# Performance work log

Hardware: AMD Instinct MI355X
Metric: run time of the kernel (lower is better)

## Reference

```python
import jax, jax.numpy as jnp
import numpy as np

V, E, H = 32000, 1024, 1024  # vocab, wemb, enc
T1, B = 129, 64


def setup_inputs() -> dict:
    key = jax.random.key(0)
    ks = jax.random.split(key, 6)
    sH = 1.0 / np.sqrt(H)
    data = jax.random.randint(ks[0], (T1, B), 0, V)
    mask = jnp.ones((T1, B), jnp.float32)
    emb = jax.random.normal(ks[1], (V, E), jnp.float32) * 0.02
    W_ih = jax.random.normal(ks[2], (E, 4 * H), jnp.float32) * sH
    W_hh = jax.random.normal(ks[3], (H, 4 * H), jnp.float32) * sH
    b = jnp.zeros((4 * H,), jnp.float32)
    Wr = jax.random.normal(ks[4], (E, H), jnp.float32) * sH  # readout: Linear(H -> E), torch weight (out,in)
    br = jnp.zeros((E,), jnp.float32)
    bd = jnp.zeros((V,), jnp.float32)  # decoder bias (weight tied to emb)
    return {"data": data, "mask": mask, "emb": emb, "W_ih": W_ih, "W_hh": W_hh,
            "b": b, "Wr": Wr, "br": br, "bd": bd}


def reference(data, mask, emb, W_ih, W_hh, b, Wr, br, bd):
    x_data = data[:-1]          # [Tx, B]
    y_data = data[1:]           # [Tx, B]
    m_all = mask[1:]            # note: source uses mask[1:] for BOTH x_mask and y_mask
    Tx, Bn = x_data.shape

    def step(carry, xs):
        ht, ct, loss = carry
        tx, ty, mt = xs                      # [B], [B], [B]
        x = emb[tx]                          # [B, E] embedding lookup
        g = x @ W_ih + ht @ W_hh + b         # [B, 4H]
        i, f, gg, o = jnp.split(g, 4, axis=1)
        i = jax.nn.sigmoid(i); f = jax.nn.sigmoid(f); o = jax.nn.sigmoid(o)
        gg = jnp.tanh(gg)
        cn = f * ct + i * gg
        hn = o * jnp.tanh(cn)
        mm = mt[:, None]
        ht2 = mm * hn + (1.0 - mm) * ht      # masked state update
        ct2 = mm * cn + (1.0 - mm) * ct
        out = ht2 @ Wr.T + br                # readout [B, E]
        logit = out @ emb.T + bd             # tied decoder [B, V]
        logp = jax.nn.log_softmax(logit, axis=1)
        nll = -jnp.take_along_axis(logp, ty[:, None], axis=1)[:, 0]
        loss = loss + jnp.mean(nll * mt)     # loss_reduction == 'org'
        return (ht2, ct2, loss), None

    init = (jnp.zeros((Bn, H), jnp.float32), jnp.zeros((Bn, H), jnp.float32),
            jnp.zeros((), jnp.float32))
    (_, _, loss), _ = jax.lax.scan(step, init, (x_data, y_data, m_all))
    return loss / Bn
```

## Files before the change

kernel.cpp:

```cpp
#include <hip/hip_runtime.h>
#include <stdint.h>

#define V_  32000
#define E_  1024
#define H_  1024
#define B_  64
#define T_  128
#define MROWS (T_ * B_)
#define NCB_ 250
#define NTG  32
#define ITEMS_PER_TG 258
#define TOTAL_ITEMS (NTG * ITEMS_PER_TG)

typedef __bf16 bf16x8 __attribute__((ext_vector_type(8)));
typedef float  f32x4  __attribute__((ext_vector_type(4)));

__device__ __forceinline__ uint16_t f2b(float f) {
  uint32_t u = __builtin_bit_cast(uint32_t, f);
  return (uint16_t)((u + 0x7fffu + ((u >> 16) & 1u)) >> 16);
}
__device__ __forceinline__ float b2f(uint16_t h) {
  uint32_t u = ((uint32_t)h) << 16;
  return __builtin_bit_cast(float, u);
}
__device__ __forceinline__ float fsig_(float x) {
  return __builtin_amdgcn_rcpf(1.0f + __expf(-x));
}
__device__ __forceinline__ float ftanh_(float x) {
  return 2.0f * __builtin_amdgcn_rcpf(1.0f + __expf(-2.0f * x)) - 1.0f;
}

__device__ __forceinline__ void gload16(const uint16_t* g, uint16_t* l) {
  __builtin_amdgcn_global_load_lds(
      (const __attribute__((address_space(1))) uint32_t*)g,
      (__attribute__((address_space(3))) uint32_t*)l,
      16, 0, 0);
}


__global__ void k_cvt(const float* __restrict__ src, uint16_t* __restrict__ dst, int n4) {
  int i = blockIdx.x * blockDim.x + threadIdx.x;
  int st = gridDim.x * blockDim.x;
  for (; i < n4; i += st) {
    float4 v = ((const float4*)src)[i];
    ushort4 o;
    o.x = f2b(v.x); o.y = f2b(v.y); o.z = f2b(v.z); o.w = f2b(v.w);
    ((ushort4*)dst)[i] = o;
  }
}

__global__ void k_tcvt(const float* __restrict__ src, uint16_t* __restrict__ dst,
                       int R, int C, int dstStride, int dstOff) {
  __shared__ float tile[32][33];
  int c0 = blockIdx.x * 32, r0 = blockIdx.y * 32;
  int tx = threadIdx.x, ty = threadIdx.y;
  for (int j = 0; j < 32; j += 8)
    tile[ty + j][tx] = src[(size_t)(r0 + ty + j) * C + c0 + tx];
  __syncthreads();
  for (int j = 0; j < 32; j += 8)
    dst[(size_t)(c0 + ty + j) * dstStride + dstOff + r0 + tx] = f2b(tile[tx][ty + j]);
}

__global__ void k_zero(uint4* p, int n) {
  int i = blockIdx.x * blockDim.x + threadIdx.x;
  int st = gridDim.x * blockDim.x;
  uint4 z = {0, 0, 0, 0};
  for (; i < n; i += st) p[i] = z;
}

__global__ __launch_bounds__(256) void k_xw(
    const int* __restrict__ data, const uint16_t* __restrict__ embB,
    const uint16_t* __restrict__ Wcat,
    const float* __restrict__ bias, uint16_t* __restrict__ xAll)
{
  __shared__ uint16_t lA[128 * 64];
  __shared__ uint16_t lB[128 * 64];

  int tid = threadIdx.x;
  int w = tid >> 6, l = tid & 63, lr = l & 15, lg = l >> 4;
  int wr = w >> 1, wc = w & 1;
  int m0 = blockIdx.x * 128;
  int n0 = blockIdx.y * 128;

  int stRow = l >> 3;
  int kswz  = ((l & 7) * 8) ^ ((stRow & 7) << 3);
  const uint16_t* aSrc[4];
  const uint16_t* bSrc[4];
#pragma unroll
  for (int cc = 0; cc < 4; ++cc) {
    int tok = data[m0 + w * 32 + cc * 8 + stRow];
    aSrc[cc] = embB + (size_t)tok * 1024 + kswz;
    bSrc[cc] = Wcat + (size_t)(n0 + w * 32 + cc * 8 + stRow) * 2048 + kswz;
  }

  f32x4 acc[4][4] = {};

  for (int kt = 0; kt < 1024; kt += 64) {
#pragma unroll
    for (int cc = 0; cc < 4; ++cc) {
      gload16(aSrc[cc] + kt, &lA[(w * 4 + cc) * 512]);
      gload16(bSrc[cc] + kt, &lB[(w * 4 + cc) * 512]);
    }
    __syncthreads();
#pragma unroll
    for (int ksub = 0; ksub < 2; ++ksub) {
      bf16x8 af[4], bfr[4];
      int ke = ksub * 32 + lg * 8;
#pragma unroll
      for (int mi = 0; mi < 4; ++mi) {
        int row = wr * 64 + mi * 16 + lr;
        af[mi] = *(const bf16x8*)&lA[row * 64 + (ke ^ ((row & 7) << 3))];
      }
#pragma unroll
      for (int ni = 0; ni < 4; ++ni) {
        int row = wc * 64 + ni * 16 + lr;
        bfr[ni] = *(const bf16x8*)&lB[row * 64 + (ke ^ ((row & 7) << 3))];
      }
#pragma unroll
      for (int mi = 0; mi < 4; ++mi)
#pragma unroll
        for (int ni = 0; ni < 4; ++ni)
          acc[mi][ni] = __builtin_amdgcn_mfma_f32_16x16x32_bf16(af[mi], bfr[ni], acc[mi][ni], 0, 0, 0);
    }
    __syncthreads();
  }

  float bv[4];
#pragma unroll
  for (int ni = 0; ni < 4; ++ni) bv[ni] = bias[n0 + wc * 64 + ni * 16 + lr];
#pragma unroll
  for (int mi = 0; mi < 4; ++mi)
#pragma unroll
    for (int ni = 0; ni < 4; ++ni) {
      int row = wr * 64 + mi * 16 + lg * 4;
      int col = n0 + wc * 64 + ni * 16 + lr;
#pragma unroll
      for (int r = 0; r < 4; ++r)
        xAll[(size_t)(m0 + row + r) * 4096 + col] = f2b(acc[mi][ni][r] + bv[ni]);
    }
}

__global__ __launch_bounds__(512) void k_mega(
    const uint16_t* __restrict__ xAll, const uint16_t* __restrict__ Wcat,
    const float* __restrict__ mask, uint16_t* __restrict__ hAll,
    uint32_t* __restrict__ flags,
    const uint16_t* __restrict__ embB, const uint16_t* __restrict__ WrB,
    const float* __restrict__ br, const float* __restrict__ bd,
    uint16_t* __restrict__ outAll, float2* __restrict__ part,
    uint32_t* __restrict__ projDone, uint32_t* __restrict__ workCtr)
{
  __shared__ alignas(16) char smem[151616];

  int tid = threadIdx.x;
  int blk = blockIdx.x;
  int w = tid >> 6, l = tid & 63, lr = l & 15, lg = l >> 4;

  if (blk < 64) {
    uint16_t* wh    = (uint16_t*)smem;
    uint16_t* xs0   = (uint16_t*)(smem + 131072);
    uint16_t* xs1   = (uint16_t*)(smem + 139264);
    uint16_t* hp0   = (uint16_t*)(smem + 147456);
    uint16_t* hp1   = (uint16_t*)(smem + 149504);
    uint32_t* ldsT  = (uint32_t*)(smem + 151552);
    uint16_t* xsb[2] = {xs0, xs1};
    uint16_t* hpb[2] = {hp0, hp1};

    int u0 = blk * 16;

    for (int it = 0; it < 16; ++it) {
      int ch = it * 512 + tid;
      int c  = ch >> 7;
      int kb = (ch & 127) * 16;
      int gRow = (c & 3) * 1024 + u0 + (c >> 2);
      uint4 v = *(const uint4*)((const char*)Wcat + (size_t)gRow * 4096 + 2048 + kb);
      *(uint4*)((char*)wh + c * 2048 + (kb ^ ((c & 7) << 4))) = v;
    }

    int wm = w >> 1, wn = w & 1;
    int q = lr & 3;

    const char* wb0 = (const char*)wh + (size_t)(wn * 32 + lr) * 2048;
    const char* wb1 = (const char*)wh + (size_t)(wn * 32 + 16 + lr) * 2048;
    int xr = (lr & 7) << 4;

    int sRow = tid >> 3, sQ = (tid >> 1) & 3, sHalf = tid & 1;
    const uint16_t* xSrc = xAll + (size_t)sRow * 4096 + sQ * 1024 + u0 + sHalf * 8;
    int xDstOff = sRow * 64 + sQ * 16 + sHalf * 8;
    int xoBase = (wm * 16 + lg * 4) * 64 + q * 16 + wn * 8 + (lr >> 2);

    float cR[2][4] = {}, hR[2][4] = {};

    if (tid == 0) *ldsT = 0;
    *(uint4*)&xsb[0][xDstOff] = *(const uint4*)xSrc;
    __syncthreads();

    int cur = 0;
    for (int t = 0; t < T_; ++t) {
      float xwv[2][4], mm_[4];
#pragma unroll
      for (int ni = 0; ni < 2; ++ni)
#pragma unroll
        for (int r = 0; r < 4; ++r)
          xwv[ni][r] = b2f(xsb[cur][xoBase + r * 64 + ni * 4]);
#pragma unroll
      for (int r = 0; r < 4; ++r)
        mm_[r] = mask[(t + 1) * B_ + wm * 16 + lg * 4 + r];

      if (t + 1 < T_)
        *(uint4*)&xsb[cur ^ 1][xDstOff] = *(const uint4*)(xSrc + (size_t)(t + 1) * B_ * 4096);

      if (t > 0) {
        uint32_t tv = (uint32_t)t;
        if (w == 0) {
          while (!__all((int)(__hip_atomic_load(&flags[l], __ATOMIC_RELAXED,
                                                __HIP_MEMORY_SCOPE_AGENT) >= tv)))
            __builtin_amdgcn_s_sleep(1);
          __hip_atomic_store(ldsT, tv, __ATOMIC_RELEASE, __HIP_MEMORY_SCOPE_WORKGROUP);
        } else {
          while (__hip_atomic_load(ldsT, __ATOMIC_ACQUIRE,
                                   __HIP_MEMORY_SCOPE_WORKGROUP) < tv)
            __builtin_amdgcn_s_sleep(1);
        }
        asm volatile("" ::: "memory");
      }

      const uint16_t* aH = hAll + (size_t)t * (B_ * H_) + (size_t)(wm * 16 + lr) * H_ + lg * 8;

      f32x4 acc0 = {0.f, 0.f, 0.f, 0.f}, acc1 = {0.f, 0.f, 0.f, 0.f};
#pragma unroll 8
      for (int ks = 0; ks < 32; ++ks) {
        bf16x8 a = *(const bf16x8*)(aH + ks * 32);
        int ko = (ks * 64 + lg * 16) ^ xr;
        bf16x8 b0 = *(const bf16x8*)(wb0 + ko);
        bf16x8 b1 = *(const bf16x8*)(wb1 + ko);
        acc0 = __builtin_amdgcn_mfma_f32_16x16x32_bf16(a, b0, acc0, 0, 0, 0);
        acc1 = __builtin_amdgcn_mfma_f32_16x16x32_bf16(a, b1, acc1, 0, 0, 0);
      }

#pragma unroll
      for (int ni = 0; ni < 2; ++ni) {
        f32x4 accv = ni ? acc1 : acc0;
#pragma unroll
        for (int r = 0; r < 4; ++r) {
          float v0 = accv[r] + xwv[ni][r];
          float v1 = __shfl_xor(v0, 1, 64);
          float v2 = __shfl_xor(v0, 2, 64);
          float v3 = __shfl_xor(v0, 3, 64);
          float gi = (q == 0) ? v0 : (q == 1) ? v1 : (q == 2) ? v2 : v3;
          float gf = (q == 1) ? v0 : (q == 0) ? v1 : (q == 3) ? v2 : v3;
          float gg = (q == 2) ? v0 : (q == 3) ? v1 : (q == 0) ? v2 : v3;
          float go = (q == 3) ? v0 : (q == 2) ? v1 : (q == 1) ? v2 : v3;
          gi = fsig_(gi); gf = fsig_(gf); gg = ftanh_(gg); go = fsig_(go);
          float cn = gf * cR[ni][r] + gi * gg;
          float hn = go * ftanh_(cn);
          float mm = mm_[r];
          cR[ni][r] = mm * cn + (1.f - mm) * cR[ni][r];
          hR[ni][r] = mm * hn + (1.f - mm) * hR[ni][r];
          if (q == 0)
            hpb[cur][(wm * 16 + lg * 4 + r) * 16 + wn * 8 + ni * 4 + (lr >> 2)] = f2b(hR[ni][r]);
        }
      }

      __syncthreads();

      if (w == 0) {
        const unsigned long long* hp = (const unsigned long long*)hpb[cur];
        unsigned long long* hd =
            (unsigned long long*)(hAll + (size_t)(t + 1) * (B_ * H_) + (size_t)l * H_ + u0);
#pragma unroll
        for (int j = 0; j < 4; ++j)
          __hip_atomic_store(hd + j, hp[l * 4 + j],
                             __ATOMIC_RELAXED, __HIP_MEMORY_SCOPE_AGENT);
        asm volatile("s_waitcnt vmcnt(0)" ::: "memory");
        if (l == 0)
          __hip_atomic_store(&flags[blk], (uint32_t)(t + 1),
                             __ATOMIC_RELAXED, __HIP_MEMORY_SCOPE_AGENT);
      }
      cur ^= 1;
    }
  } else {
    uint16_t* lA  = (uint16_t*)smem;
    uint16_t* lB  = (uint16_t*)(smem + 32768);
    float2*   cm  = (float2*)(smem + 49152);
    uint32_t* sId = (uint32_t*)(smem + 53248);

    int stRow = l >> 3;
    int kswz  = ((l & 7) * 8) ^ ((stRow & 7) << 3);
    int wr = w >> 1;
    int wc = w & 1;

    for (;;) {
      __syncthreads();
      if (tid == 0)
        *sId = __hip_atomic_fetch_add(workCtr, 1u, __ATOMIC_RELAXED, __HIP_MEMORY_SCOPE_AGENT);
      __syncthreads();
      uint32_t id = *sId;
      if (id >= TOTAL_ITEMS) break;
      int tg = (int)(id / ITEMS_PER_TG), sub = (int)(id % ITEMS_PER_TG);
      int t0 = tg * 4;
      bool isProj = (sub < 8);

      const uint16_t* Abase;
      const uint16_t* Bbase;
      const float* biasp;
      if (isProj) {
        uint32_t tv = (uint32_t)(t0 + 4);
        while (!__all((int)(__hip_atomic_load(&flags[l], __ATOMIC_RELAXED,
                                              __HIP_MEMORY_SCOPE_AGENT) >= tv)))
          __builtin_amdgcn_s_sleep(8);
        asm volatile("" ::: "memory");
        Abase = hAll + (size_t)(t0 + 1) * (B_ * H_);
        Bbase = WrB + (size_t)(sub * 128) * 1024;
        biasp = br + sub * 128;
      } else {
        while (__hip_atomic_load(&projDone[tg], __ATOMIC_RELAXED,
                                 __HIP_MEMORY_SCOPE_AGENT) < 8u)
          __builtin_amdgcn_s_sleep(8);
        asm volatile("" ::: "memory");
        Abase = outAll + (size_t)t0 * B_ * 1024;
        Bbase = embB + (size_t)(sub - 8) * 128 * 1024;
        biasp = bd + (sub - 8) * 128;
      }

      const uint16_t* aS = Abase + (size_t)(w * 32 + stRow) * 1024 + kswz;
      const uint16_t* bS = Bbase + (size_t)(w * 16 + stRow) * 1024 + kswz;

      f32x4 acc[4][4] = {};
      for (int kt = 0; kt < 1024; kt += 64) {
#pragma unroll
        for (int cc = 0; cc < 4; ++cc)
          gload16(aS + (size_t)cc * 8 * 1024 + kt, &lA[(w * 4 + cc) * 512]);
#pragma unroll
        for (int cc = 0; cc < 2; ++cc)
          gload16(bS + (size_t)cc * 8 * 1024 + kt, &lB[(w * 2 + cc) * 512]);
        __syncthreads();
#pragma unroll
        for (int ksub = 0; ksub < 2; ++ksub) {
          int ke = ksub * 32 + lg * 8;
          bf16x8 af[4], bfr[4];
#pragma unroll
          for (int mi = 0; mi < 4; ++mi) {
            int row = wr * 64 + mi * 16 + lr;
            af[mi] = *(const bf16x8*)&lA[row * 64 + (ke ^ ((row & 7) << 3))];
          }
#pragma unroll
          for (int ni = 0; ni < 4; ++ni) {
            int row = wc * 64 + ni * 16 + lr;
            bfr[ni] = *(const bf16x8*)&lB[row * 64 + (ke ^ ((row & 7) << 3))];
          }
#pragma unroll
          for (int mi = 0; mi < 4; ++mi)
#pragma unroll
            for (int ni = 0; ni < 4; ++ni)
              acc[mi][ni] = __builtin_amdgcn_mfma_f32_16x16x32_bf16(af[mi], bfr[ni], acc[mi][ni], 0, 0, 0);
        }
        __syncthreads();
      }

      float bv[4];
#pragma unroll
      for (int ni = 0; ni < 4; ++ni) bv[ni] = biasp[wc * 64 + ni * 16 + lr];

      if (isProj) {
        int e0 = sub * 128;
        uint16_t* opack = lA;
#pragma unroll
        for (int chunk = 0; chunk < 4; ++chunk) {
          if (wr == chunk) {
#pragma unroll
            for (int mi = 0; mi < 4; ++mi)
#pragma unroll
              for (int ni = 0; ni < 4; ++ni)
#pragma unroll
                for (int r = 0; r < 4; ++r)
                  opack[(mi * 16 + lg * 4 + r) * 128 + wc * 64 + ni * 16 + lr]
                    = f2b(acc[mi][ni][r] + bv[ni]);
          }
          __syncthreads();
          const unsigned long long* op = (const unsigned long long*)opack;
#pragma unroll
          for (int j = 0; j < 4; ++j) {
            int g = j * 512 + tid;
            int row = g >> 5, seg = g & 31;
            unsigned long long* od =
                (unsigned long long*)(outAll + ((size_t)(t0 + chunk) * B_ + row) * 1024 + e0) + seg;
            __hip_atomic_store(od, op[g], __ATOMIC_RELAXED, __HIP_MEMORY_SCOPE_AGENT);
          }
          __syncthreads();
        }
        asm volatile("s_waitcnt vmcnt(0)" ::: "memory");
        __syncthreads();
        if (tid == 0)
          __hip_atomic_fetch_add(&projDone[tg], 1u, __ATOMIC_RELAXED, __HIP_MEMORY_SCOPE_AGENT);
      } else {
        int nc = sub - 8;
#pragma unroll
        for (int mi = 0; mi < 4; ++mi) {
#pragma unroll
          for (int r = 0; r < 4; ++r) {
            float mx = -1e30f;
#pragma unroll
            for (int ni = 0; ni < 4; ++ni) { acc[mi][ni][r] += bv[ni]; mx = fmaxf(mx, acc[mi][ni][r]); }
#pragma unroll
            for (int d = 1; d < 16; d <<= 1) mx = fmaxf(mx, __shfl_xor(mx, d, 64));
            float s = 0.f;
#pragma unroll
            for (int ni = 0; ni < 4; ++ni) s += expf(acc[mi][ni][r] - mx);
#pragma unroll
            for (int d = 1; d < 16; d <<= 1) s += __shfl_xor(s, d, 64);
            if (lr == 0) cm[wc * 256 + wr * 64 + mi * 16 + lg * 4 + r] = make_float2(mx, s);
          }
        }
        __syncthreads();
        if (tid < 256) {
          float2 p0 = cm[tid], p1 = cm[256 + tid];
          float M = fmaxf(p0.x, p1.x);
          float S = p0.y * expf(p0.x - M) + p1.y * expf(p1.x - M);
          part[(size_t)nc * MROWS + (size_t)t0 * B_ + tid] = make_float2(M, S);
        }
      }
    }
  }
}

__global__ __launch_bounds__(256) void k_tgt(
    const uint16_t* __restrict__ outAll, const uint16_t* __restrict__ embB,
    const float* __restrict__ bd, const int* __restrict__ data, float* __restrict__ tgt)
{
  int w = threadIdx.x >> 6, l = threadIdx.x & 63;
  int row = blockIdx.x * 4 + w;
  int t = row >> 6, b = row & 63;
  int ty = data[(t + 1) * B_ + b];
  const uint16_t* a = outAll + (size_t)row * E_;
  const uint16_t* e = embB + (size_t)ty * E_;
  float s = 0.f;
#pragma unroll
  for (int i0 = 0; i0 < 2; ++i0) {
    int i = (l + i0 * 64) * 8;
    bf16x8 av = *(const bf16x8*)(a + i);
    bf16x8 ev = *(const bf16x8*)(e + i);
#pragma unroll
    for (int j = 0; j < 8; ++j) s += (float)av[j] * (float)ev[j];
  }
#pragma unroll
  for (int d = 1; d < 64; d <<= 1) s += __shfl_xor(s, d, 64);
  if (l == 0) tgt[row] = s + bd[ty];
}

__global__ __launch_bounds__(256) void k_lse(
    const float2* __restrict__ part, const float* __restrict__ tgt,
    const float* __restrict__ mask, float* __restrict__ rowNll)
{
  int w = threadIdx.x >> 6, l = threadIdx.x & 63;
  int row = blockIdx.x * 4 + w;
  float m = -1e30f, s = 0.f;
  for (int cc = l; cc < NCB_; cc += 64) {
    float2 v = part[(size_t)cc * MROWS + row];
    float M = fmaxf(m, v.x);
    s = s * expf(m - M) + v.y * expf(v.x - M);
    m = M;
  }
#pragma unroll
  for (int d = 1; d < 64; d <<= 1) {
    float om = __shfl_xor(m, d, 64);
    float os = __shfl_xor(s, d, 64);
    float M = fmaxf(m, om);
    s = s * expf(m - M) + os * expf(om - M);
    m = M;
  }
  if (l == 0) {
    int t = row >> 6, b = row & 63;
    float nll = (m + logf(s)) - tgt[row];
    rowNll[row] = nll * mask[(t + 1) * B_ + b];
  }
}

__global__ void k_final2(const float* __restrict__ rowNll, float* __restrict__ out) {
  __shared__ float red[256];
  float s = 0.f;
  for (int i = threadIdx.x; i < MROWS; i += 256) s += rowNll[i];
  red[threadIdx.x] = s;
  __syncthreads();
  for (int st = 128; st > 0; st >>= 1) {
    if ((int)threadIdx.x < st) red[threadIdx.x] += red[threadIdx.x + st];
    __syncthreads();
  }
  if (threadIdx.x == 0) out[0] = red[0] / (float)(B_ * B_);
}

extern "C" void kernel_launch(void* const* d_in, const int* in_sizes, int n_in,
                              void* d_out, int out_size, void* d_ws, size_t ws_size,
                              hipStream_t stream)
{
  const int*   data = (const int*)  d_in[0];
  const float* mask = (const float*)d_in[1];
  const float* emb  = (const float*)d_in[2];
  const float* W_ih = (const float*)d_in[3];
  const float* W_hh = (const float*)d_in[4];
  const float* bias = (const float*)d_in[5];
  const float* Wr   = (const float*)d_in[6];
  const float* br   = (const float*)d_in[7];
  const float* bd   = (const float*)d_in[8];
  (void)in_sizes; (void)n_in; (void)out_size; (void)ws_size;

  char* ws = (char*)d_ws;
  size_t off = 0;
  auto alloc = [&](size_t bytes) -> char* {
    char* p = ws + off;
    off += (bytes + 255) & ~(size_t)255;
    return p;
  };
  uint16_t* embB   = (uint16_t*)alloc((size_t)V_ * E_ * 2);
  uint16_t* Wcat   = (uint16_t*)alloc((size_t)4 * H_ * 2048 * 2);
  uint16_t* WrB    = (uint16_t*)alloc((size_t)E_ * H_ * 2);
  uint16_t* hAll   = (uint16_t*)alloc((size_t)(T_ + 1) * B_ * H_ * 2);
  uint16_t* xAll   = (uint16_t*)alloc((size_t)MROWS * 4096 * 2);
  uint16_t* outAll = (uint16_t*)alloc((size_t)MROWS * E_ * 2);
  float2*   part   = (float2*)  alloc((size_t)NCB_ * MROWS * 8);
  float*    tgt    = (float*)   alloc((size_t)MROWS * 4);
  float*    rowNll = (float*)   alloc((size_t)MROWS * 4);
  uint32_t* syncb  = (uint32_t*)alloc(4096);
  uint32_t* flags    = syncb;
  uint32_t* projDone = syncb + 128;
  uint32_t* workCtr  = syncb + 512;

  k_cvt <<<2048, 256, 0, stream>>>(emb, embB, V_ * E_ / 4);
  k_cvt <<<256,  256, 0, stream>>>(Wr, WrB, E_ * H_ / 4);
  k_tcvt<<<dim3(4 * H_ / 32, E_ / 32), dim3(32, 8), 0, stream>>>(W_ih, Wcat, E_, 4 * H_, 2048, 0);
  k_tcvt<<<dim3(4 * H_ / 32, H_ / 32), dim3(32, 8), 0, stream>>>(W_hh, Wcat, H_, 4 * H_, 2048, 1024);
  k_zero<<<32, 256, 0, stream>>>((uint4*)hAll, B_ * H_ * 2 / 16);
  k_zero<<<1, 256, 0, stream>>>((uint4*)syncb, 4096 / 16);

  k_xw<<<dim3(MROWS / 128, 4096 / 128), 256, 0, stream>>>(data, embB, Wcat, bias, xAll);

  k_mega<<<256, 512, 0, stream>>>(xAll, Wcat, mask, hAll, flags,
                                  embB, WrB, br, bd, outAll, part,
                                  projDone, workCtr);

  k_tgt   <<<MROWS / 4, 256, 0, stream>>>(outAll, embB, bd, data, tgt);
  k_lse   <<<MROWS / 4, 256, 0, stream>>>(part, tgt, mask, rowNll);
  k_final2<<<1, 256, 0, stream>>>(rowNll, (float*)d_out);
}
```

Baseline: 1.957 ms.

## Fold input-projection GEMM into persistent megakernel as overlapped work items

Removes the separate k_xw launch and turns the x@W_ih projection into 1024 work items, each covering 256 rows by 128 columns, pulled from the megakernel's work queue ahead of the readout and decoder items. Recurrent blocks wait on per-group xwDone counters before loading each group of four timesteps' inputs, so the recurrence can start once the first group is ready instead of after the whole GEMM. Projection items now wait on a single minStep word that block 0 publishes, rather than each polling all 64 flags. The cost is more spin-waiting and the risk of stalls if the queue order delays the early x-projection groups.

Measured after the change: 1.977 ms. About the same (+1.0%).

```diff
diff --git a/kernel.cpp b/kernel.cpp
--- a/kernel.cpp
+++ b/kernel.cpp
@@ -9,8 +9,9 @@
 #define MROWS (T_ * B_)
 #define NCB_ 250
 #define NTG  32
+#define NXW  1024
 #define ITEMS_PER_TG 258
-#define TOTAL_ITEMS (NTG * ITEMS_PER_TG)
+#define TOTAL_ITEMS (NXW + NTG * ITEMS_PER_TG)
 
 typedef __bf16 bf16x8 __attribute__((ext_vector_type(8)));
 typedef float  f32x4  __attribute__((ext_vector_type(4)));
@@ -68,86 +69,17 @@
   for (; i < n; i += st) p[i] = z;
 }
 
-__global__ __launch_bounds__(256) void k_xw(
-    const int* __restrict__ data, const uint16_t* __restrict__ embB,
+__global__ __launch_bounds__(512) void k_mega(
+    const int* __restrict__ data,
+    const uint16_t* __restrict__ xAllR, uint16_t* __restrict__ xAllW,
     const uint16_t* __restrict__ Wcat,
-    const float* __restrict__ bias, uint16_t* __restrict__ xAll)
-{
-  __shared__ uint16_t lA[128 * 64];
-  __shared__ uint16_t lB[128 * 64];
-
-  int tid = threadIdx.x;
-  int w = tid >> 6, l = tid & 63, lr = l & 15, lg = l >> 4;
-  int wr = w >> 1, wc = w & 1;
-  int m0 = blockIdx.x * 128;
-  int n0 = blockIdx.y * 128;
-
-  int stRow = l >> 3;
-  int kswz  = ((l & 7) * 8) ^ ((stRow & 7) << 3);
-  const uint16_t* aSrc[4];
-  const uint16_t* bSrc[4];
-#pragma unroll
-  for (int cc = 0; cc < 4; ++cc) {
-    int tok = data[m0 + w * 32 + cc * 8 + stRow];
-    aSrc[cc] = embB + (size_t)tok * 1024 + kswz;
-    bSrc[cc] = Wcat + (size_t)(n0 + w * 32 + cc * 8 + stRow) * 2048 + kswz;
-  }
-
-  f32x4 acc[4][4] = {};
-
-  for (int kt = 0; kt < 1024; kt += 64) {
-#pragma unroll
-    for (int cc = 0; cc < 4; ++cc) {
-      gload16(aSrc[cc] + kt, &lA[(w * 4 + cc) * 512]);
-      gload16(bSrc[cc] + kt, &lB[(w * 4 + cc) * 512]);
-    }
-    __syncthreads();
-#pragma unroll
-    for (int ksub = 0; ksub < 2; ++ksub) {
-      bf16x8 af[4], bfr[4];
-      int ke = ksub * 32 + lg * 8;
-#pragma unroll
-      for (int mi = 0; mi < 4; ++mi) {
-        int row = wr * 64 + mi * 16 + lr;
-        af[mi] = *(const bf16x8*)&lA[row * 64 + (ke ^ ((row & 7) << 3))];
-      }
-#pragma unroll
-      for (int ni = 0; ni < 4; ++ni) {
-        int row = wc * 64 + ni * 16 + lr;
-        bfr[ni] = *(const bf16x8*)&lB[row * 64 + (ke ^ ((row & 7) << 3))];
-      }
-#pragma unroll
-      for (int mi = 0; mi < 4; ++mi)
-#pragma unroll
-        for (int ni = 0; ni < 4; ++ni)
-          acc[mi][ni] = __builtin_amdgcn_mfma_f32_16x16x32_bf16(af[mi], bfr[ni], acc[mi][ni], 0, 0, 0);
-    }
-    __syncthreads();
-  }
-
-  float bv[4];
-#pragma unroll
-  for (int ni = 0; ni < 4; ++ni) bv[ni] = bias[n0 + wc * 64 + ni * 16 + lr];
-#pragma unroll
-  for (int mi = 0; mi < 4; ++mi)
-#pragma unroll
-    for (int ni = 0; ni < 4; ++ni) {
-      int row = wr * 64 + mi * 16 + lg * 4;
-      int col = n0 + wc * 64 + ni * 16 + lr;
-#pragma unroll
-      for (int r = 0; r < 4; ++r)
-        xAll[(size_t)(m0 + row + r) * 4096 + col] = f2b(acc[mi][ni][r] + bv[ni]);
-    }
-}
-
-__global__ __launch_bounds__(512) void k_mega(
-    const uint16_t* __restrict__ xAll, const uint16_t* __restrict__ Wcat,
-    const float* __restrict__ mask, uint16_t* __restrict__ hAll,
-    uint32_t* __restrict__ flags,
+    const float* __restrict__ bias, const float* __restrict__ mask,
+    uint16_t* __restrict__ hAll, uint32_t* __restrict__ flags,
     const uint16_t* __restrict__ embB, const uint16_t* __restrict__ WrB,
     const float* __restrict__ br, const float* __restrict__ bd,
     uint16_t* __restrict__ outAll, float2* __restrict__ part,
-    uint32_t* __restrict__ projDone, uint32_t* __restrict__ workCtr)
+    uint32_t* __restrict__ projDone, uint32_t* __restrict__ xwDone,
+    uint32_t* __restrict__ minStep, uint32_t* __restrict__ workCtr)
 {
   __shared__ alignas(16) char smem[151616];
 
@@ -184,13 +116,16 @@
     int xr = (lr & 7) << 4;
 
     int sRow = tid >> 3, sQ = (tid >> 1) & 3, sHalf = tid & 1;
-    const uint16_t* xSrc = xAll + (size_t)sRow * 4096 + sQ * 1024 + u0 + sHalf * 8;
+    const uint16_t* xSrc = xAllR + (size_t)sRow * 4096 + sQ * 1024 + u0 + sHalf * 8;
     int xDstOff = sRow * 64 + sQ * 16 + sHalf * 8;
     int xoBase = (wm * 16 + lg * 4) * 64 + q * 16 + wn * 8 + (lr >> 2);
 
     float cR[2][4] = {}, hR[2][4] = {};
 
     if (tid == 0) *ldsT = 0;
+    while (__hip_atomic_load(&xwDone[0], __ATOMIC_RELAXED, __HIP_MEMORY_SCOPE_AGENT) < 32u)
+      __builtin_amdgcn_s_sleep(8);
+    asm volatile("" ::: "memory");
     *(uint4*)&xsb[0][xDstOff] = *(const uint4*)xSrc;
     __syncthreads();
 
@@ -206,8 +141,16 @@
       for (int r = 0; r < 4; ++r)
         mm_[r] = mask[(t + 1) * B_ + wm * 16 + lg * 4 + r];
 
-      if (t + 1 < T_)
+      if (t + 1 < T_) {
+        if (((t + 1) & 3) == 0) {
+          uint32_t g = (uint32_t)((t + 1) >> 2);
+          while (__hip_atomic_load(&xwDone[g], __ATOMIC_RELAXED,
+                                   __HIP_MEMORY_SCOPE_AGENT) < 32u)
+            __builtin_amdgcn_s_sleep(8);
+          asm volatile("" ::: "memory");
+        }
         *(uint4*)&xsb[cur ^ 1][xDstOff] = *(const uint4*)(xSrc + (size_t)(t + 1) * B_ * 4096);
+      }
 
       if (t > 0) {
         uint32_t tv = (uint32_t)t;
@@ -216,6 +159,8 @@
                                                 __HIP_MEMORY_SCOPE_AGENT) >= tv)))
             __builtin_amdgcn_s_sleep(1);
           __hip_atomic_store(ldsT, tv, __ATOMIC_RELEASE, __HIP_MEMORY_SCOPE_WORKGROUP);
+          if (blk == 0 && l == 0)
+            __hip_atomic_store(minStep, tv, __ATOMIC_RELAXED, __HIP_MEMORY_SCOPE_AGENT);
         } else {
           while (__hip_atomic_load(ldsT, __ATOMIC_ACQUIRE,
                                    __HIP_MEMORY_SCOPE_WORKGROUP) < tv)
@@ -278,6 +223,14 @@
       }
       cur ^= 1;
     }
+
+    if (blk == 0 && w == 0) {
+      while (!__all((int)(__hip_atomic_load(&flags[l], __ATOMIC_RELAXED,
+                                            __HIP_MEMORY_SCOPE_AGENT) >= (uint32_t)T_)))
+        __builtin_amdgcn_s_sleep(1);
+      if (l == 0)
+        __hip_atomic_store(minStep, (uint32_t)T_, __ATOMIC_RELAXED, __HIP_MEMORY_SCOPE_AGENT);
+    }
   } else {
     uint16_t* lA  = (uint16_t*)smem;
     uint16_t* lB  = (uint16_t*)(smem + 32768);
@@ -296,43 +249,65 @@
       __syncthreads();
       uint32_t id = *sId;
       if (id >= TOTAL_ITEMS) break;
-      int tg = (int)(id / ITEMS_PER_TG), sub = (int)(id % ITEMS_PER_TG);
+
+      int itemType;
+      int tg = 0, sub = 0, rgx = 0, cgx = 0;
+      if (id < NXW) {
+        itemType = 0; rgx = (int)(id >> 5); cgx = (int)(id & 31);
+      } else {
+        int id2 = (int)(id - NXW);
+        tg = id2 / ITEMS_PER_TG; sub = id2 % ITEMS_PER_TG;
+        itemType = (sub < 8) ? 1 : 2;
+      }
       int t0 = tg * 4;
-      bool isProj = (sub < 8);
-
-      const uint16_t* Abase;
-      const uint16_t* Bbase;
+
+      const uint16_t* aSrc[4];
+      const uint16_t* bS;
       const float* biasp;
-      if (isProj) {
-        uint32_t tv = (uint32_t)(t0 + 4);
-        while (!__all((int)(__hip_atomic_load(&flags[l], __ATOMIC_RELAXED,
-                                              __HIP_MEMORY_SCOPE_AGENT) >= tv)))
-          __builtin_amdgcn_s_sleep(8);
+      int bStride;
+      if (itemType == 0) {
+#pragma unroll
+        for (int cc = 0; cc < 4; ++cc) {
+          int row = rgx * 256 + w * 32 + cc * 8 + stRow;
+          aSrc[cc] = embB + (size_t)data[row] * 1024 + kswz;
+        }
+        bS = Wcat + (size_t)(cgx * 128 + w * 16 + stRow) * 2048 + kswz;
+        biasp = bias + cgx * 128;
+        bStride = 2048;
+      } else if (itemType == 1) {
+        while (__hip_atomic_load(minStep, __ATOMIC_RELAXED,
+                                 __HIP_MEMORY_SCOPE_AGENT) < (uint32_t)(t0 + 4))
+          __builtin_amdgcn_s_sleep(16);
         asm volatile("" ::: "memory");
-        Abase = hAll + (size_t)(t0 + 1) * (B_ * H_);
-        Bbase = WrB + (size_t)(sub * 128) * 1024;
+        const uint16_t* Abase = hAll + (size_t)(t0 + 1) * (B_ * H_);
+#pragma unroll
+        for (int cc = 0; cc < 4; ++cc)
+          aSrc[cc] = Abase + (size_t)(w * 32 + cc * 8 + stRow) * 1024 + kswz;
+        bS = WrB + (size_t)(sub * 128 + w * 16 + stRow) * 1024 + kswz;
         biasp = br + sub * 128;
+        bStride = 1024;
       } else {
         while (__hip_atomic_load(&projDone[tg], __ATOMIC_RELAXED,
                                  __HIP_MEMORY_SCOPE_AGENT) < 8u)
-          __builtin_amdgcn_s_sleep(8);
+          __builtin_amdgcn_s_sleep(16);
         asm volatile("" ::: "memory");
-        Abase = outAll + (size_t)t0 * B_ * 1024;
-        Bbase = embB + (size_t)(sub - 8) * 128 * 1024;
+        const uint16_t* Abase = outAll + (size_t)t0 * B_ * 1024;
+#pragma unroll
+        for (int cc = 0; cc < 4; ++cc)
+          aSrc[cc] = Abase + (size_t)(w * 32 + cc * 8 + stRow) * 1024 + kswz;
+        bS = embB + (size_t)((sub - 8) * 128 + w * 16 + stRow) * 1024 + kswz;
         biasp = bd + (sub - 8) * 128;
-      }
-
-      const uint16_t* aS = Abase + (size_t)(w * 32 + stRow) * 1024 + kswz;
-      const uint16_t* bS = Bbase + (size_t)(w * 16 + stRow) * 1024 + kswz;
+        bStride = 1024;
+      }
 
       f32x4 acc[4][4] = {};
       for (int kt = 0; kt < 1024; kt += 64) {
 #pragma unroll
         for (int cc = 0; cc < 4; ++cc)
-          gload16(aS + (size_t)cc * 8 * 1024 + kt, &lA[(w * 4 + cc) * 512]);
+          gload16(aSrc[cc] + (size_t)cc * 0 + (size_t)kt, &lA[(w * 4 + cc) * 512]);
 #pragma unroll
         for (int cc = 0; cc < 2; ++cc)
-          gload16(bS + (size_t)cc * 8 * 1024 + kt, &lB[(w * 2 + cc) * 512]);
+          gload16(bS + (size_t)cc * 8 * bStride + kt, &lB[(w * 2 + cc) * 512]);
         __syncthreads();
 #pragma unroll
         for (int ksub = 0; ksub < 2; ++ksub) {
@@ -361,8 +336,8 @@
 #pragma unroll
       for (int ni = 0; ni < 4; ++ni) bv[ni] = biasp[wc * 64 + ni * 16 + lr];
 
-      if (isProj) {
-        int e0 = sub * 128;
+      if (itemType == 0) {
+        int n0 = cgx * 128;
         uint16_t* opack = lA;
 #pragma unroll
         for (int chunk = 0; chunk < 4; ++chunk) {
@@ -380,11 +355,42 @@
           const unsigned long long* op = (const unsigned long long*)opack;
 #pragma unroll
           for (int j = 0; j < 4; ++j) {
-            int g = j * 512 + tid;
-            int row = g >> 5, seg = g & 31;
+            int g2 = j * 512 + tid;
+            int row = g2 >> 5, seg = g2 & 31;
+            unsigned long long* od =
+                (unsigned long long*)(xAllW + (size_t)(rgx * 256 + chunk * 64 + row) * 4096 + n0) + seg;
+            __hip_atomic_store(od, op[g2], __ATOMIC_RELAXED, __HIP_MEMORY_SCOPE_AGENT);
+          }
+          __syncthreads();
+        }
+        asm volatile("s_waitcnt vmcnt(0)" ::: "memory");
+        __syncthreads();
+        if (tid == 0)
+          __hip_atomic_fetch_add(&xwDone[rgx], 1u, __ATOMIC_RELAXED, __HIP_MEMORY_SCOPE_AGENT);
+      } else if (itemType == 1) {
+        int e0 = sub * 128;
+        uint16_t* opack = lA;
+#pragma unroll
+        for (int chunk = 0; chunk < 4; ++chunk) {
+          if (wr == chunk) {
+#pragma unroll
+            for (int mi = 0; mi < 4; ++mi)
+#pragma unroll
+              for (int ni = 0; ni < 4; ++ni)
+#pragma unroll
+                for (int r = 0; r < 4; ++r)
+                  opack[(mi * 16 + lg * 4 + r) * 128 + wc * 64 + ni * 16 + lr]
+                    = f2b(acc[mi][ni][r] + bv[ni]);
+          }
+          __syncthreads();
+          const unsigned long long* op = (const unsigned long long*)opack;
+#pragma unroll
+          for (int j = 0; j < 4; ++j) {
+            int g2 = j * 512 + tid;
+            int row = g2 >> 5, seg = g2 & 31;
             unsigned long long* od =
                 (unsigned long long*)(outAll + ((size_t)(t0 + chunk) * B_ + row) * 1024 + e0) + seg;
-            __hip_atomic_store(od, op[g], __ATOMIC_RELAXED, __HIP_MEMORY_SCOPE_AGENT);
+            __hip_atomic_store(od, op[g2], __ATOMIC_RELAXED, __HIP_MEMORY_SCOPE_AGENT);
           }
           __syncthreads();
         }
@@ -522,7 +528,9 @@
   uint32_t* syncb  = (uint32_t*)alloc(4096);
   uint32_t* flags    = syncb;
   uint32_t* projDone = syncb + 128;
+  uint32_t* xwDone   = syncb + 192;
   uint32_t* workCtr  = syncb + 512;
+  uint32_t* minStep  = syncb + 576;
 
   k_cvt <<<2048, 256, 0, stream>>>(emb, embB, V_ * E_ / 4);
   k_cvt <<<256,  256, 0, stream>>>(Wr, WrB, E_ * H_ / 4);
@@ -531,11 +539,9 @@
   k_zero<<<32, 256, 0, stream>>>((uint4*)hAll, B_ * H_ * 2 / 16);
   k_zero<<<1, 256, 0, stream>>>((uint4*)syncb, 4096 / 16);
 
-  k_xw<<<dim3(MROWS / 128, 4096 / 128), 256, 0, stream>>>(data, embB, Wcat, bias, xAll);
-
-  k_mega<<<256, 512, 0, stream>>>(xAll, Wcat, mask, hAll, flags,
+  k_mega<<<256, 512, 0, stream>>>(data, xAll, xAll, Wcat, bias, mask, hAll, flags,
                                   embB, WrB, br, bd, outAll, part,
-                                  projDone, workCtr);
+                                  projDone, xwDone, minStep, workCtr);
 
   k_tgt   <<<MROWS / 4, 256, 0, stream>>>(outAll, embB, bd, data, tgt);
   k_lse   <<<MROWS / 4, 256, 0, stream>>>(part, tgt, mask, rowNll);
```
